# Kernel optimization log

Measured on AMD Instinct MI355X. Metric: run time of the kernel, lower is better.

The kernel has to match this reference:

```python
import jax, jax.numpy as jnp
import numpy as np

N_NODES = 50000
N_EDGES = 600000
N_GRAPHS = 64
D_IN = 128
D_HID = 128
D_LAT = 64
BN_EPS = 1e-5


def setup_inputs() -> dict:
    key = jax.random.key(0)
    ks = jax.random.split(key, 8)
    x = jax.random.normal(ks[0], (N_NODES, D_IN), dtype=jnp.float32)
    edge_index = jax.random.randint(ks[1], (2, N_EDGES), 0, N_NODES, dtype=jnp.int64 if jax.config.jax_enable_x64 else jnp.int32)
    batch = jnp.sort(jax.random.randint(ks[2], (N_NODES,), 0, N_GRAPHS))
    d_cat = 13 * D_IN  # x + (mean,max,min,std) x (identity,amp,att)
    s = 1.0 / np.sqrt(d_cat)
    W0 = jax.random.normal(ks[3], (d_cat, D_HID), dtype=jnp.float32) * s
    W1 = jax.random.normal(ks[4], (13 * D_HID, D_HID), dtype=jnp.float32) * s
    W2 = jax.random.normal(ks[5], (13 * D_HID, D_HID), dtype=jnp.float32) * s
    fcW = jax.random.normal(ks[6], (D_HID, D_LAT), dtype=jnp.float32) * (1.0 / np.sqrt(D_HID))
    return {
        "x": x, "edge_index": edge_index, "batch": batch,
        "W0": W0, "b0": jnp.zeros((D_HID,), jnp.float32),
        "W1": W1, "b1": jnp.zeros((D_HID,), jnp.float32),
        "W2": W2, "b2": jnp.zeros((D_HID,), jnp.float32),
        "bn_gamma": jnp.ones((D_HID,), jnp.float32),
        "bn_beta": jnp.zeros((D_HID,), jnp.float32),
        "fcW": fcW, "fcb": jnp.zeros((D_LAT,), jnp.float32),
    }


def _pna_conv(h, W, b, src, dst, deg, delta):
    # h: [N, d]; messages gathered from source nodes per edge: [E, d]
    m = h[src]
    cnt = jnp.maximum(deg, 1.0)[:, None]
    ssum = jax.ops.segment_sum(m, dst, num_segments=N_NODES)
    mean = ssum / cnt
    ssq = jax.ops.segment_sum(m * m, dst, num_segments=N_NODES)
    std = jnp.sqrt(jnp.maximum(ssq / cnt - mean * mean, 0.0) + 1e-5)
    mx = jax.ops.segment_max(m, dst, num_segments=N_NODES)
    mn = jax.ops.segment_min(m, dst, num_segments=N_NODES)
    has = (deg > 0)[:, None]
    mx = jnp.where(has, mx, 0.0)
    mn = jnp.where(has, mn, 0.0)
    agg = jnp.concatenate([mean, mx, mn, std], axis=-1)  # [N, 4d]
    logd = jnp.log(deg + 1.0)[:, None]
    amp = logd / delta
    att = delta / jnp.maximum(logd, 1e-5)
    feat = jnp.concatenate([h, agg, agg * amp, agg * att], axis=-1)  # [N, 13d]
    return feat @ W + b


def reference(x, edge_index, batch, W0, b0, W1, b1, W2, b2, bn_gamma, bn_beta, fcW, fcb):
    src, dst = edge_index[0], edge_index[1]
    deg = jax.ops.segment_sum(jnp.ones((src.shape[0],), x.dtype), dst, num_segments=N_NODES)
    delta = jnp.mean(jnp.log(deg + 1.0))  # avg log-degree normalizer
    h = jax.nn.relu(_pna_conv(x, W0, b0, src, dst, deg, delta))
    h = jax.nn.relu(_pna_conv(h, W1, b1, src, dst, deg, delta))
    h = jax.nn.relu(_pna_conv(h, W2, b2, src, dst, deg, delta))
    # dropout is identity in eval mode
    pooled = jax.ops.segment_sum(h, batch, num_segments=N_GRAPHS)  # global_add_pool
    mu = jnp.mean(pooled, axis=0)
    var = jnp.var(pooled, axis=0)
    bn = (pooled - mu) / jnp.sqrt(var + BN_EPS) * bn_gamma + bn_beta
    return bn @ fcW + fcb
```

## Files before the change

kernel.cpp:

```cpp
#include <hip/hip_runtime.h>
#include <cstdint>
#include <cstddef>

#define N_NODESC 50000
#define N_PAD    50048
#define N_EDGESC 600000
#define N_GRAPHSC 64
#define D_HIDC   128
#define D_LATC   64
#define D_GS     512
#define D_WROW   1664

typedef unsigned short u16;
typedef unsigned int   u32;

typedef _Float16 f16x8 __attribute__((ext_vector_type(8)));
typedef _Float16 f16x2 __attribute__((ext_vector_type(2)));
typedef float    f32x4 __attribute__((ext_vector_type(4)));
typedef float    f32x2 __attribute__((ext_vector_type(2)));

__device__ __forceinline__ u16 f2h(float f) {
    return __builtin_bit_cast(u16, (_Float16)f);
}
__device__ __forceinline__ float h2f(u16 u) {
    return (float)__builtin_bit_cast(_Float16, u);
}

__device__ __forceinline__ f32x2 pk_add(f32x2 a, f32x2 b) {
    f32x2 d;
    asm("v_pk_add_f32 %0, %1, %2" : "=v"(d) : "v"(a), "v"(b));
    return d;
}
__device__ __forceinline__ f32x2 pk_fma(f32x2 a, f32x2 b, f32x2 c) {
    f32x2 d;
    asm("v_pk_fma_f32 %0, %1, %2, %3" : "=v"(d) : "v"(a), "v"(b), "v"(c));
    return d;
}

__device__ __forceinline__ void gll16(void* lds, const void* g) {
    __builtin_amdgcn_global_load_lds(
        (const __attribute__((address_space(1))) void*)g,
        (__attribute__((address_space(3))) void*)lds, 16, 0, 0);
}

__global__ void __launch_bounds__(256) k_setup(
        const float* __restrict__ x, const float* __restrict__ W0,
        const float* __restrict__ W1, const float* __restrict__ W2,
        const int* __restrict__ batch,
        u16* __restrict__ h, u16* __restrict__ Wt,
        int* __restrict__ zero_base, int nz, int ZB, int* __restrict__ goff) {
    int b = blockIdx.x;
    int t = threadIdx.x;
    if (b < ZB) {
        int i = b * 256 + t;
        if (i < nz) zero_base[i] = 0;
        return;
    }
    b -= ZB;
    if (b < 12500) {
        int i = b * 256 + t;
        float2 v = ((const float2*)x)[i];
        ((u32*)h)[i] = (u32)f2h(v.x) | ((u32)f2h(v.y) << 16);
        return;
    }
    b -= 12500;
    if (b < 2496) {
        int which = b / 832;
        int i = (b % 832) * 256 + t;
        const float* W = (which == 0) ? W0 : (which == 1) ? W1 : W2;
        int k = i / D_HIDC, j = i % D_HIDC;
        Wt[(size_t)which * D_WROW * D_HIDC + (size_t)j * D_WROW + k] = f2h(W[i]);
        return;
    }
    int g = t;
    if (g <= N_GRAPHSC) {
        int lo = 0, hi = N_NODESC;
        while (lo < hi) {
            int mid = (lo + hi) >> 1;
            if (batch[mid] < g) lo = mid + 1; else hi = mid;
        }
        goff[g] = lo;
    }
}

__global__ void k_count(const int* __restrict__ dst, int* __restrict__ deg) {
    int e = blockIdx.x * 256 + threadIdx.x;
    if (e < N_EDGESC) atomicAdd(&deg[dst[e]], 1);
}

__global__ void __launch_bounds__(256) k_scan_part(
        const int* __restrict__ deg, int* __restrict__ bsum,
        float* __restrict__ lsum) {
    __shared__ int s[256];
    __shared__ float ls[256];
    int idx = blockIdx.x * 256 + threadIdx.x;
    int v = (idx < N_NODESC) ? deg[idx] : 0;
    s[threadIdx.x] = v;
    ls[threadIdx.x] = (idx < N_NODESC) ? logf((float)v + 1.0f) : 0.0f;
    __syncthreads();
    for (int o = 128; o > 0; o >>= 1) {
        if (threadIdx.x < o) {
            s[threadIdx.x] += s[threadIdx.x + o];
            ls[threadIdx.x] += ls[threadIdx.x + o];
        }
        __syncthreads();
    }
    if (threadIdx.x == 0) { bsum[blockIdx.x] = s[0]; lsum[blockIdx.x] = ls[0]; }
}

__global__ void __launch_bounds__(256) k_scan_block(
        int* __restrict__ bsum, const float* __restrict__ lsum,
        float* __restrict__ delta_p) {
    __shared__ int s[256];
    __shared__ float ls[256];
    int t = threadIdx.x;
    int v = (t < 196) ? bsum[t] : 0;
    s[t] = v;
    ls[t] = (t < 196) ? lsum[t] : 0.0f;
    __syncthreads();
    for (int o = 1; o < 256; o <<= 1) {
        int add = (t >= o) ? s[t - o] : 0;
        __syncthreads();
        s[t] += add;
        __syncthreads();
    }
    if (t < 196) bsum[t] = s[t] - v;
    for (int o = 128; o > 0; o >>= 1) {
        if (t < o) ls[t] += ls[t + o];
        __syncthreads();
    }
    if (t == 0) delta_p[0] = ls[0] * (1.0f / (float)N_NODESC);
}

__global__ void __launch_bounds__(256) k_scan_final(
        const int* __restrict__ deg, const int* __restrict__ bsum,
        int* __restrict__ row_off) {
    __shared__ int s[256];
    int t = threadIdx.x;
    int idx = blockIdx.x * 256 + t;
    int v = (idx < N_NODESC) ? deg[idx] : 0;
    s[t] = v; __syncthreads();
    for (int o = 1; o < 256; o <<= 1) {
        int add = (t >= o) ? s[t - o] : 0;
        __syncthreads();
        s[t] += add;
        __syncthreads();
    }
    int excl = s[t] - v + bsum[blockIdx.x];
    if (idx < N_NODESC) row_off[idx] = excl;
    if (idx == 0) row_off[N_NODESC] = N_EDGESC;
}

__global__ void k_fill_csr(const int* __restrict__ src, const int* __restrict__ dst,
                           const int* __restrict__ row_off, int* __restrict__ cursor,
                           int* __restrict__ csr_src) {
    int e = blockIdx.x * 256 + threadIdx.x;
    if (e < N_EDGESC) {
        int d = dst[e];
        int pos = row_off[d] + atomicAdd(&cursor[d], 1);
        csr_src[pos] = src[e] << 8;
    }
}


__global__ void __launch_bounds__(256) k_aggregate(
        const u16* __restrict__ h, const int* __restrict__ row_off,
        const int* __restrict__ csr_src, u16* __restrict__ G) {
    int n = blockIdx.x * 4 + (threadIdx.x >> 6);
    if (n >= N_NODESC) return;
    int lane = threadIdx.x & 63;
    int half = lane >> 5, l32 = lane & 31;
    int c4 = 4 * l32;
    u32 c8 = 8u * (u32)l32;
    const char* h8 = (const char*)h;
    int beg = row_off[n], end = row_off[n + 1];
    const _Float16 NEG = (_Float16)(-65504.0f), POS = (_Float16)(65504.0f);
    f32x2 s01 = {0.f, 0.f}, s23 = {0.f, 0.f};
    f32x2 q01 = {0.f, 0.f}, q23 = {0.f, 0.f};
    f16x2 mx01 = {NEG, NEG}, mx23 = {NEG, NEG};
    f16x2 mn01 = {POS, POS}, mn23 = {POS, POS};

    #define PROC(u) { \
        f16x2 p01 = __builtin_bit_cast(f16x2, (u).x); \
        f16x2 p23 = __builtin_bit_cast(f16x2, (u).y); \
        f32x2 c01 = __builtin_convertvector(p01, f32x2); \
        f32x2 c23 = __builtin_convertvector(p23, f32x2); \
        s01 = pk_add(s01, c01); s23 = pk_add(s23, c23); \
        q01 = pk_fma(c01, c01, q01); q23 = pk_fma(c23, c23, q23); \
        mx01 = __builtin_elementwise_max(mx01, p01); \
        mx23 = __builtin_elementwise_max(mx23, p23); \
        mn01 = __builtin_elementwise_min(mn01, p01); \
        mn23 = __builtin_elementwise_min(mn23, p23); }

    int i = beg + half;
    for (; i + 6 < end; i += 8) {
        u32 e0 = (u32)csr_src[i],     e1 = (u32)csr_src[i + 2];
        u32 e2 = (u32)csr_src[i + 4], e3 = (u32)csr_src[i + 6];
        uint2 u0 = *(const uint2*)(h8 + (e0 + c8));
        uint2 u1 = *(const uint2*)(h8 + (e1 + c8));
        uint2 u2 = *(const uint2*)(h8 + (e2 + c8));
        uint2 u3 = *(const uint2*)(h8 + (e3 + c8));
        PROC(u0); PROC(u1); PROC(u2); PROC(u3);
    }
    for (; i < end; i += 2) {
        u32 e0 = (u32)csr_src[i];
        uint2 u0 = *(const uint2*)(h8 + (e0 + c8));
        PROC(u0);
    }
    #undef PROC

    s01.x += __shfl_xor(s01.x, 32); s01.y += __shfl_xor(s01.y, 32);
    s23.x += __shfl_xor(s23.x, 32); s23.y += __shfl_xor(s23.y, 32);
    q01.x += __shfl_xor(q01.x, 32); q01.y += __shfl_xor(q01.y, 32);
    q23.x += __shfl_xor(q23.x, 32); q23.y += __shfl_xor(q23.y, 32);
    #define MRG(v, OP) v = OP(v, \
        __builtin_bit_cast(f16x2, __shfl_xor(__builtin_bit_cast(int, v), 32)))
    MRG(mx01, __builtin_elementwise_max); MRG(mx23, __builtin_elementwise_max);
    MRG(mn01, __builtin_elementwise_min); MRG(mn23, __builtin_elementwise_min);
    #undef MRG

    int d = end - beg;
    float inv = 1.0f / fmaxf((float)d, 1.0f);
    float me0 = s01.x * inv, me1 = s01.y * inv;
    float me2 = s23.x * inv, me3 = s23.y * inv;
    float sd0 = sqrtf(fmaxf(q01.x * inv - me0 * me0, 0.0f) + 1e-5f);
    float sd1 = sqrtf(fmaxf(q01.y * inv - me1 * me1, 0.0f) + 1e-5f);
    float sd2 = sqrtf(fmaxf(q23.x * inv - me2 * me2, 0.0f) + 1e-5f);
    float sd3 = sqrtf(fmaxf(q23.y * inv - me3 * me3, 0.0f) + 1e-5f);
    float fx0 = (float)mx01.x, fx1 = (float)mx01.y;
    float fx2 = (float)mx23.x, fx3 = (float)mx23.y;
    float fn0 = (float)mn01.x, fn1 = (float)mn01.y;
    float fn2 = (float)mn23.x, fn3 = (float)mn23.y;
    if (d == 0) {
        fx0 = fx1 = fx2 = fx3 = 0.0f;
        fn0 = fn1 = fn2 = fn3 = 0.0f;
    }
    u16* base = G + (size_t)n * D_GS;
    #define PK2(a, b) ((u32)f2h(a) | ((u32)f2h(b) << 16))
    if (half == 0) {
        uint2 m; m.x = PK2(me0, me1); m.y = PK2(me2, me3);
        *(uint2*)(base + c4) = m;
        uint2 X; X.x = PK2(fx0, fx1); X.y = PK2(fx2, fx3);
        *(uint2*)(base + 128 + c4) = X;
    } else {
        uint2 N_; N_.x = PK2(fn0, fn1); N_.y = PK2(fn2, fn3);
        *(uint2*)(base + 256 + c4) = N_;
        uint2 S; S.x = PK2(sd0, sd1); S.y = PK2(sd2, sd3);
        *(uint2*)(base + 384 + c4) = S;
    }
    #undef PK2
}

__global__ void __launch_bounds__(256, 2) k_gemm(
        const u16* __restrict__ hin, const u16* __restrict__ G,
        const u16* __restrict__ Wt,
        const int* __restrict__ deg, const float* __restrict__ delta_p,
        const float* __restrict__ bias, u16* __restrict__ hout) {
    __shared__ _Float16 A1[128 * 64];
    __shared__ _Float16 A2[128 * 64];
    __shared__ _Float16 A3[128 * 64];
    __shared__ _Float16 Bt[128 * 64];
    const _Float16* Wf = (const _Float16*)Wt;
    const _Float16* Gf = (const _Float16*)G;
    const _Float16* Hf = (const _Float16*)hin;
    int n0 = blockIdx.x * 128;
    int t = threadIdx.x;
    int w = t >> 6, lane = t & 63;
    int srow8 = lane >> 3, sslot = lane & 7;
    int stg = (sslot ^ srow8) * 8;
    int q4 = lane >> 4, r16 = lane & 15;
    int sx0 = (q4 ^ (lane & 7)) * 8;
    int sx1 = ((q4 + 4) ^ (lane & 7)) * 8;
    int col = lane & 15;

    float delta = delta_p[0];
    float atv[8];
    _Float16 amh[8];
    #pragma unroll
    for (int nt = 0; nt < 8; nt++) {
        int node = n0 + nt * 16 + col;
        float logd = logf((float)deg[node] + 1.0f);
        amh[nt] = (_Float16)(logd / delta);
        atv[nt] = delta / fmaxf(logd, 1e-5f);
    }

    f32x4 acc[2][8], ac3[2][8];
    #pragma unroll
    for (int a = 0; a < 2; a++)
        #pragma unroll
        for (int b = 0; b < 8; b++) {
            acc[a][b] = (f32x4){0.f, 0.f, 0.f, 0.f};
            ac3[a][b] = (f32x4){0.f, 0.f, 0.f, 0.f};
        }

    for (int ki = 0; ki < 10; ki++) {
        int k0 = ki * 64;
        bool sreg = (k0 >= 128);
        __syncthreads();
        #pragma unroll
        for (int r = 0; r < 4; r++) {
            int rr = r * 4 + w;
            const _Float16* wrow = Wf + (size_t)(rr * 8 + srow8) * D_WROW;
            gll16(&A1[rr * 512], wrow + k0 + stg);
        }
        if (sreg) {
            #pragma unroll
            for (int r = 0; r < 4; r++) {
                int rr = r * 4 + w;
                const _Float16* wrow = Wf + (size_t)(rr * 8 + srow8) * D_WROW;
                gll16(&A2[rr * 512], wrow + 512 + k0 + stg);
                gll16(&A3[rr * 512], wrow + 1024 + k0 + stg);
            }
        }
        #pragma unroll
        for (int q = 0; q < 4; q++) {
            int rr = q * 4 + w;
            int row = n0 + rr * 8 + srow8;
            const _Float16* bsrc = (!sreg)
                ? Hf + (size_t)row * D_HIDC + k0 + stg
                : Gf + (size_t)row * D_GS + (k0 - 128) + stg;
            gll16(&Bt[rr * 512], bsrc);
        }
        __syncthreads();
        f16x8 a00 = *(const f16x8*)&A1[(w * 32 + r16) * 64 + sx0];
        f16x8 a01 = *(const f16x8*)&A1[(w * 32 + r16) * 64 + sx1];
        f16x8 a10 = *(const f16x8*)&A1[(w * 32 + 16 + r16) * 64 + sx0];
        f16x8 a11 = *(const f16x8*)&A1[(w * 32 + 16 + r16) * 64 + sx1];
        if (!sreg) {
            #pragma unroll
            for (int nt = 0; nt < 8; nt++) {
                f16x8 b0 = *(const f16x8*)&Bt[(nt * 16 + r16) * 64 + sx0];
                f16x8 b1 = *(const f16x8*)&Bt[(nt * 16 + r16) * 64 + sx1];
                acc[0][nt] = __builtin_amdgcn_mfma_f32_16x16x32_f16(a00, b0, acc[0][nt], 0, 0, 0);
                acc[1][nt] = __builtin_amdgcn_mfma_f32_16x16x32_f16(a10, b0, acc[1][nt], 0, 0, 0);
                acc[0][nt] = __builtin_amdgcn_mfma_f32_16x16x32_f16(a01, b1, acc[0][nt], 0, 0, 0);
                acc[1][nt] = __builtin_amdgcn_mfma_f32_16x16x32_f16(a11, b1, acc[1][nt], 0, 0, 0);
            }
        } else {
            f16x8 w2a0 = *(const f16x8*)&A2[(w * 32 + r16) * 64 + sx0];
            f16x8 w2a1 = *(const f16x8*)&A2[(w * 32 + r16) * 64 + sx1];
            f16x8 w2b0 = *(const f16x8*)&A2[(w * 32 + 16 + r16) * 64 + sx0];
            f16x8 w2b1 = *(const f16x8*)&A2[(w * 32 + 16 + r16) * 64 + sx1];
            f16x8 w3a0 = *(const f16x8*)&A3[(w * 32 + r16) * 64 + sx0];
            f16x8 w3a1 = *(const f16x8*)&A3[(w * 32 + r16) * 64 + sx1];
            f16x8 w3b0 = *(const f16x8*)&A3[(w * 32 + 16 + r16) * 64 + sx0];
            f16x8 w3b1 = *(const f16x8*)&A3[(w * 32 + 16 + r16) * 64 + sx1];
            #pragma unroll
            for (int nt = 0; nt < 8; nt++) {
                f16x8 b0 = *(const f16x8*)&Bt[(nt * 16 + r16) * 64 + sx0];
                f16x8 b1 = *(const f16x8*)&Bt[(nt * 16 + r16) * 64 + sx1];
                f16x8 bm0 = b0 * amh[nt];
                f16x8 bm1 = b1 * amh[nt];
                acc[0][nt] = __builtin_amdgcn_mfma_f32_16x16x32_f16(a00, b0, acc[0][nt], 0, 0, 0);
                acc[1][nt] = __builtin_amdgcn_mfma_f32_16x16x32_f16(a10, b0, acc[1][nt], 0, 0, 0);
                acc[0][nt] = __builtin_amdgcn_mfma_f32_16x16x32_f16(a01, b1, acc[0][nt], 0, 0, 0);
                acc[1][nt] = __builtin_amdgcn_mfma_f32_16x16x32_f16(a11, b1, acc[1][nt], 0, 0, 0);
                acc[0][nt] = __builtin_amdgcn_mfma_f32_16x16x32_f16(w2a0, bm0, acc[0][nt], 0, 0, 0);
                acc[1][nt] = __builtin_amdgcn_mfma_f32_16x16x32_f16(w2b0, bm0, acc[1][nt], 0, 0, 0);
                acc[0][nt] = __builtin_amdgcn_mfma_f32_16x16x32_f16(w2a1, bm1, acc[0][nt], 0, 0, 0);
                acc[1][nt] = __builtin_amdgcn_mfma_f32_16x16x32_f16(w2b1, bm1, acc[1][nt], 0, 0, 0);
                ac3[0][nt] = __builtin_amdgcn_mfma_f32_16x16x32_f16(w3a0, b0, ac3[0][nt], 0, 0, 0);
                ac3[1][nt] = __builtin_amdgcn_mfma_f32_16x16x32_f16(w3b0, b0, ac3[1][nt], 0, 0, 0);
                ac3[0][nt] = __builtin_amdgcn_mfma_f32_16x16x32_f16(w3a1, b1, ac3[0][nt], 0, 0, 0);
                ac3[1][nt] = __builtin_amdgcn_mfma_f32_16x16x32_f16(w3b1, b1, ac3[1][nt], 0, 0, 0);
            }
        }
    }
    int rowq = q4 * 4;
    #pragma unroll
    for (int nt = 0; nt < 8; nt++) {
        int node = n0 + nt * 16 + col;
        float at = atv[nt];
        #pragma unroll
        for (int mt = 0; mt < 2; mt++) {
            int jb = w * 32 + mt * 16 + rowq;
            f32x4 v = acc[mt][nt], v3 = ac3[mt][nt];
            ushort4 o;
            o.x = f2h(fmaxf(v.x + at * v3.x + bias[jb], 0.0f));
            o.y = f2h(fmaxf(v.y + at * v3.y + bias[jb + 1], 0.0f));
            o.z = f2h(fmaxf(v.z + at * v3.z + bias[jb + 2], 0.0f));
            o.w = f2h(fmaxf(v.w + at * v3.w + bias[jb + 3], 0.0f));
            *(ushort4*)&hout[(size_t)node * D_HIDC + jb] = o;
        }
    }
}


__global__ void __launch_bounds__(256) k_pool(
        const u16* __restrict__ h, const int* __restrict__ goff,
        float* __restrict__ pooled) {
    __shared__ float sm[256];
    int g = blockIdx.x >> 2, s = blockIdx.x & 3;
    int gb = goff[g], ge = goff[g + 1];
    int len = ge - gb;
    int q = (len + 3) >> 2;
    int nb = gb + s * q;
    int ne = min(nb + q, ge);
    int t = threadIdx.x;
    int j = t & 127, half = t >> 7;
    float acc = 0.0f;
    for (int n = nb + half; n < ne; n += 2)
        acc += h2f(h[(size_t)n * D_HIDC + j]);
    sm[t] = acc; __syncthreads();
    if (t < 128) {
        float v = sm[t] + sm[t + 128];
        atomicAdd(&pooled[g * D_HIDC + j], v);
    }
}

__global__ void __launch_bounds__(128) k_bn_fc(
        const float* __restrict__ pooled, const float* __restrict__ gamma,
        const float* __restrict__ beta, const float* __restrict__ fcW,
        const float* __restrict__ fcb, float* __restrict__ out) {
    __shared__ float bn[D_HIDC];
    int g = blockIdx.x, t = threadIdx.x;
    float s = 0.f, q = 0.f;
    for (int gg = 0; gg < N_GRAPHSC; gg++) {
        float v = pooled[gg * D_HIDC + t];
        s += v; q += v * v;
    }
    float mu = s * (1.0f / N_GRAPHSC);
    float var = q * (1.0f / N_GRAPHSC) - mu * mu;
    float inv = 1.0f / sqrtf(var + 1e-5f);
    bn[t] = (pooled[g * D_HIDC + t] - mu) * inv * gamma[t] + beta[t];
    __syncthreads();
    if (t < D_LATC) {
        float accum = fcb[t];
        for (int j = 0; j < D_HIDC; j++) accum += bn[j] * fcW[j * D_LATC + t];
        out[g * D_LATC + t] = accum;
    }
}


extern "C" void kernel_launch(void* const* d_in, const int* in_sizes, int n_in,
                              void* d_out, int out_size, void* d_ws, size_t ws_size,
                              hipStream_t stream) {
    const float* x     = (const float*)d_in[0];
    const int*   ei    = (const int*)d_in[1];
    const int*   batch = (const int*)d_in[2];
    const float* W0 = (const float*)d_in[3];
    const float* b0 = (const float*)d_in[4];
    const float* W1 = (const float*)d_in[5];
    const float* b1 = (const float*)d_in[6];
    const float* W2 = (const float*)d_in[7];
    const float* b2 = (const float*)d_in[8];
    const float* gamma = (const float*)d_in[9];
    const float* beta  = (const float*)d_in[10];
    const float* fcW   = (const float*)d_in[11];
    const float* fcb   = (const float*)d_in[12];
    float* out = (float*)d_out;
    const int* srcv = ei;
    const int* dstv = ei + N_EDGESC;

    char* p = (char*)d_ws;
    auto alloc = [&](size_t bytes) -> char* {
        char* r = p;
        p += (bytes + 255) & ~(size_t)255;
        return r;
    };
    int*   deg_cnt = (int*)alloc((size_t)N_PAD * 4);
    int*   cursor  = (int*)alloc((size_t)N_NODESC * 4);
    float* delta_p = (float*)alloc(4);
    float* pooled  = (float*)alloc((size_t)N_GRAPHSC * D_HIDC * 4);
    char*  zero_end = p;
    int*   row_off = (int*)alloc((size_t)(N_NODESC + 1) * 4);
    int*   goff    = (int*)alloc((size_t)(N_GRAPHSC + 1) * 4);
    int*   bsum    = (int*)alloc(256 * 4);
    float* lsum    = (float*)alloc(256 * 4);
    int*   csr_src = (int*)alloc((size_t)N_EDGESC * 4);
    u16*   Wt      = (u16*)alloc((size_t)3 * D_WROW * D_HIDC * 2);
    u16*   hA      = (u16*)alloc((size_t)N_PAD * D_HIDC * 2);
    u16*   hB      = (u16*)alloc((size_t)N_PAD * D_HIDC * 2);
    u16*   G       = (u16*)alloc((size_t)N_PAD * D_GS * 2);

    int nz = (int)((zero_end - (char*)deg_cnt) / 4);
    int ZB = (nz + 255) / 256;
    int setup_grid = ZB + 12500 + 2496 + 1;
    k_setup<<<setup_grid, 256, 0, stream>>>(x, W0, W1, W2, batch,
                                            hB, Wt, deg_cnt, nz, ZB, goff);
    k_count<<<(N_EDGESC + 255) / 256, 256, 0, stream>>>(dstv, deg_cnt);
    k_scan_part<<<196, 256, 0, stream>>>(deg_cnt, bsum, lsum);
    k_scan_block<<<1, 256, 0, stream>>>(bsum, lsum, delta_p);
    k_scan_final<<<196, 256, 0, stream>>>(deg_cnt, bsum, row_off);
    k_fill_csr<<<(N_EDGESC + 255) / 256, 256, 0, stream>>>(srcv, dstv, row_off, cursor, csr_src);

    const float* bs[3] = {b0, b1, b2};
    const u16* h_in[3]  = {hB, hA, hB};
    u16*       h_out[3] = {hA, hB, hA};
    size_t wsz = (size_t)D_WROW * D_HIDC;
    for (int l = 0; l < 3; l++) {
        k_aggregate<<<(N_NODESC + 3) / 4, 256, 0, stream>>>(
            h_in[l], row_off, csr_src, G);
        k_gemm<<<N_PAD / 128, 256, 0, stream>>>(
            h_in[l], G, Wt + (size_t)l * wsz, deg_cnt, delta_p, bs[l], h_out[l]);
    }
    k_pool<<<4 * N_GRAPHSC, 256, 0, stream>>>(h_out[2], goff, pooled);
    k_bn_fc<<<N_GRAPHSC, 128, 0, stream>>>(pooled, gamma, beta, fcW, fcb, out);
}
```

Baseline: 396.2 us.

## Double-buffer GEMM LDS tiles with async prefetch and halved K-step

The fused PNA GEMM kernel now uses two LDS buffers with 32-wide K tiles instead of one 64-wide tile. The next tile's global-to-LDS loads are issued before computing the current one, and explicit vmcnt waits plus raw barriers replace the __syncthreads pairs, so load latency overlaps MFMA work. It also raises wave priority during compute. The cost is more loop iterations and barriers, plus fragile hand-counted vmcnt values that must match the number of loads issued per stage.

```diff
diff --git a/kernel.cpp b/kernel.cpp
--- a/kernel.cpp
+++ b/kernel.cpp
@@ -256,22 +256,29 @@
         const u16* __restrict__ Wt,
         const int* __restrict__ deg, const float* __restrict__ delta_p,
         const float* __restrict__ bias, u16* __restrict__ hout) {
-    __shared__ _Float16 A1[128 * 64];
-    __shared__ _Float16 A2[128 * 64];
-    __shared__ _Float16 A3[128 * 64];
-    __shared__ _Float16 Bt[128 * 64];
+    __shared__ _Float16 A1[2][128 * 32];
+    __shared__ _Float16 A2[2][128 * 32];
+    __shared__ _Float16 A3[2][128 * 32];
+    __shared__ _Float16 Bt[2][128 * 32];
     const _Float16* Wf = (const _Float16*)Wt;
     const _Float16* Gf = (const _Float16*)G;
     const _Float16* Hf = (const _Float16*)hin;
     int n0 = blockIdx.x * 128;
     int t = threadIdx.x;
     int w = t >> 6, lane = t & 63;
-    int srow8 = lane >> 3, sslot = lane & 7;
-    int stg = (sslot ^ srow8) * 8;
+    int srow4 = lane >> 2, schk = lane & 3;
+    int scol = (schk ^ (srow4 & 3)) * 8;
     int q4 = lane >> 4, r16 = lane & 15;
-    int sx0 = (q4 ^ (lane & 7)) * 8;
-    int sx1 = ((q4 + 4) ^ (lane & 7)) * 8;
-    int col = lane & 15;
+    int sx = (q4 ^ (r16 & 3)) * 8;
+    int col = r16;
+    int iA0 = w, iA1 = 4 + w;
+
+    const _Float16* wA0 = Wf + (size_t)(iA0 * 16 + srow4) * D_WROW + scol;
+    const _Float16* wA1 = Wf + (size_t)(iA1 * 16 + srow4) * D_WROW + scol;
+    const _Float16* hB0 = Hf + (size_t)(n0 + iA0 * 16 + srow4) * D_HIDC + scol;
+    const _Float16* hB1 = Hf + (size_t)(n0 + iA1 * 16 + srow4) * D_HIDC + scol;
+    const _Float16* gB0 = Gf + (size_t)(n0 + iA0 * 16 + srow4) * D_GS + scol - 128;
+    const _Float16* gB1 = Gf + (size_t)(n0 + iA1 * 16 + srow4) * D_GS + scol - 128;
 
     float delta = delta_p[0];
     float atv[8];
@@ -293,79 +300,69 @@
             ac3[a][b] = (f32x4){0.f, 0.f, 0.f, 0.f};
         }
 
-    for (int ki = 0; ki < 10; ki++) {
-        int k0 = ki * 64;
-        bool sreg = (k0 >= 128);
-        __syncthreads();
-        #pragma unroll
-        for (int r = 0; r < 4; r++) {
-            int rr = r * 4 + w;
-            const _Float16* wrow = Wf + (size_t)(rr * 8 + srow8) * D_WROW;
-            gll16(&A1[rr * 512], wrow + k0 + stg);
-        }
-        if (sreg) {
-            #pragma unroll
-            for (int r = 0; r < 4; r++) {
-                int rr = r * 4 + w;
-                const _Float16* wrow = Wf + (size_t)(rr * 8 + srow8) * D_WROW;
-                gll16(&A2[rr * 512], wrow + 512 + k0 + stg);
-                gll16(&A3[rr * 512], wrow + 1024 + k0 + stg);
-            }
-        }
-        #pragma unroll
-        for (int q = 0; q < 4; q++) {
-            int rr = q * 4 + w;
-            int row = n0 + rr * 8 + srow8;
-            const _Float16* bsrc = (!sreg)
-                ? Hf + (size_t)row * D_HIDC + k0 + stg
-                : Gf + (size_t)row * D_GS + (k0 - 128) + stg;
-            gll16(&Bt[rr * 512], bsrc);
-        }
-        __syncthreads();
-        f16x8 a00 = *(const f16x8*)&A1[(w * 32 + r16) * 64 + sx0];
-        f16x8 a01 = *(const f16x8*)&A1[(w * 32 + r16) * 64 + sx1];
-        f16x8 a10 = *(const f16x8*)&A1[(w * 32 + 16 + r16) * 64 + sx0];
-        f16x8 a11 = *(const f16x8*)&A1[(w * 32 + 16 + r16) * 64 + sx1];
-        if (!sreg) {
-            #pragma unroll
-            for (int nt = 0; nt < 8; nt++) {
-                f16x8 b0 = *(const f16x8*)&Bt[(nt * 16 + r16) * 64 + sx0];
-                f16x8 b1 = *(const f16x8*)&Bt[(nt * 16 + r16) * 64 + sx1];
-                acc[0][nt] = __builtin_amdgcn_mfma_f32_16x16x32_f16(a00, b0, acc[0][nt], 0, 0, 0);
-                acc[1][nt] = __builtin_amdgcn_mfma_f32_16x16x32_f16(a10, b0, acc[1][nt], 0, 0, 0);
-                acc[0][nt] = __builtin_amdgcn_mfma_f32_16x16x32_f16(a01, b1, acc[0][nt], 0, 0, 0);
-                acc[1][nt] = __builtin_amdgcn_mfma_f32_16x16x32_f16(a11, b1, acc[1][nt], 0, 0, 0);
-            }
-        } else {
-            f16x8 w2a0 = *(const f16x8*)&A2[(w * 32 + r16) * 64 + sx0];
-            f16x8 w2a1 = *(const f16x8*)&A2[(w * 32 + r16) * 64 + sx1];
-            f16x8 w2b0 = *(const f16x8*)&A2[(w * 32 + 16 + r16) * 64 + sx0];
-            f16x8 w2b1 = *(const f16x8*)&A2[(w * 32 + 16 + r16) * 64 + sx1];
-            f16x8 w3a0 = *(const f16x8*)&A3[(w * 32 + r16) * 64 + sx0];
-            f16x8 w3a1 = *(const f16x8*)&A3[(w * 32 + r16) * 64 + sx1];
-            f16x8 w3b0 = *(const f16x8*)&A3[(w * 32 + 16 + r16) * 64 + sx0];
-            f16x8 w3b1 = *(const f16x8*)&A3[(w * 32 + 16 + r16) * 64 + sx1];
-            #pragma unroll
-            for (int nt = 0; nt < 8; nt++) {
-                f16x8 b0 = *(const f16x8*)&Bt[(nt * 16 + r16) * 64 + sx0];
-                f16x8 b1 = *(const f16x8*)&Bt[(nt * 16 + r16) * 64 + sx1];
-                f16x8 bm0 = b0 * amh[nt];
-                f16x8 bm1 = b1 * amh[nt];
-                acc[0][nt] = __builtin_amdgcn_mfma_f32_16x16x32_f16(a00, b0, acc[0][nt], 0, 0, 0);
-                acc[1][nt] = __builtin_amdgcn_mfma_f32_16x16x32_f16(a10, b0, acc[1][nt], 0, 0, 0);
-                acc[0][nt] = __builtin_amdgcn_mfma_f32_16x16x32_f16(a01, b1, acc[0][nt], 0, 0, 0);
-                acc[1][nt] = __builtin_amdgcn_mfma_f32_16x16x32_f16(a11, b1, acc[1][nt], 0, 0, 0);
-                acc[0][nt] = __builtin_amdgcn_mfma_f32_16x16x32_f16(w2a0, bm0, acc[0][nt], 0, 0, 0);
-                acc[1][nt] = __builtin_amdgcn_mfma_f32_16x16x32_f16(w2b0, bm0, acc[1][nt], 0, 0, 0);
-                acc[0][nt] = __builtin_amdgcn_mfma_f32_16x16x32_f16(w2a1, bm1, acc[0][nt], 0, 0, 0);
-                acc[1][nt] = __builtin_amdgcn_mfma_f32_16x16x32_f16(w2b1, bm1, acc[1][nt], 0, 0, 0);
-                ac3[0][nt] = __builtin_amdgcn_mfma_f32_16x16x32_f16(w3a0, b0, ac3[0][nt], 0, 0, 0);
-                ac3[1][nt] = __builtin_amdgcn_mfma_f32_16x16x32_f16(w3b0, b0, ac3[1][nt], 0, 0, 0);
-                ac3[0][nt] = __builtin_amdgcn_mfma_f32_16x16x32_f16(w3a1, b1, ac3[0][nt], 0, 0, 0);
-                ac3[1][nt] = __builtin_amdgcn_mfma_f32_16x16x32_f16(w3b1, b1, ac3[1][nt], 0, 0, 0);
-            }
-        }
-    }
+    #define STAGE(KI, BUF) do { \
+        gll16(&A1[BUF][iA0 * 512], wA0 + (KI) * 32); \
+        gll16(&A1[BUF][iA1 * 512], wA1 + (KI) * 32); \
+        if ((KI) >= 4) { \
+            gll16(&A2[BUF][iA0 * 512], wA0 + 512 + (KI) * 32); \
+            gll16(&A2[BUF][iA1 * 512], wA1 + 512 + (KI) * 32); \
+            gll16(&A3[BUF][iA0 * 512], wA0 + 1024 + (KI) * 32); \
+            gll16(&A3[BUF][iA1 * 512], wA1 + 1024 + (KI) * 32); \
+            gll16(&Bt[BUF][iA0 * 512], gB0 + (KI) * 32); \
+            gll16(&Bt[BUF][iA1 * 512], gB1 + (KI) * 32); \
+        } else { \
+            gll16(&Bt[BUF][iA0 * 512], hB0 + (KI) * 32); \
+            gll16(&Bt[BUF][iA1 * 512], hB1 + (KI) * 32); \
+        } \
+    } while (0)
+
+    #define COMPUTE(KI, BUF) do { \
+        f16x8 a00 = *(const f16x8*)&A1[BUF][(w * 32 + r16) * 32 + sx]; \
+        f16x8 a10 = *(const f16x8*)&A1[BUF][(w * 32 + 16 + r16) * 32 + sx]; \
+        if ((KI) < 4) { \
+            _Pragma("unroll") \
+            for (int nt = 0; nt < 8; nt++) { \
+                f16x8 b0 = *(const f16x8*)&Bt[BUF][(nt * 16 + r16) * 32 + sx]; \
+                acc[0][nt] = __builtin_amdgcn_mfma_f32_16x16x32_f16(a00, b0, acc[0][nt], 0, 0, 0); \
+                acc[1][nt] = __builtin_amdgcn_mfma_f32_16x16x32_f16(a10, b0, acc[1][nt], 0, 0, 0); \
+            } \
+        } else { \
+            f16x8 w2l = *(const f16x8*)&A2[BUF][(w * 32 + r16) * 32 + sx]; \
+            f16x8 w2h = *(const f16x8*)&A2[BUF][(w * 32 + 16 + r16) * 32 + sx]; \
+            f16x8 w3l = *(const f16x8*)&A3[BUF][(w * 32 + r16) * 32 + sx]; \
+            f16x8 w3h = *(const f16x8*)&A3[BUF][(w * 32 + 16 + r16) * 32 + sx]; \
+            _Pragma("unroll") \
+            for (int nt = 0; nt < 8; nt++) { \
+                f16x8 b0 = *(const f16x8*)&Bt[BUF][(nt * 16 + r16) * 32 + sx]; \
+                f16x8 bm = b0 * amh[nt]; \
+                acc[0][nt] = __builtin_amdgcn_mfma_f32_16x16x32_f16(a00, b0, acc[0][nt], 0, 0, 0); \
+                acc[1][nt] = __builtin_amdgcn_mfma_f32_16x16x32_f16(a10, b0, acc[1][nt], 0, 0, 0); \
+                acc[0][nt] = __builtin_amdgcn_mfma_f32_16x16x32_f16(w2l, bm, acc[0][nt], 0, 0, 0); \
+                acc[1][nt] = __builtin_amdgcn_mfma_f32_16x16x32_f16(w2h, bm, acc[1][nt], 0, 0, 0); \
+                ac3[0][nt] = __builtin_amdgcn_mfma_f32_16x16x32_f16(w3l, b0, ac3[0][nt], 0, 0, 0); \
+                ac3[1][nt] = __builtin_amdgcn_mfma_f32_16x16x32_f16(w3h, b0, ac3[1][nt], 0, 0, 0); \
+            } \
+        } \
+    } while (0)
+
+    asm volatile("s_waitcnt vmcnt(0)" ::: "memory");
+    STAGE(0, 0);
+    #pragma unroll
+    for (int ki = 0; ki < 20; ki++) {
+        int cb = ki & 1, nb = cb ^ 1;
+        if (ki < 19) STAGE(ki + 1, nb);
+        if (ki == 19)        asm volatile("s_waitcnt vmcnt(0)" ::: "memory");
+        else if (ki + 1 < 4) asm volatile("s_waitcnt vmcnt(4)" ::: "memory");
+        else                 asm volatile("s_waitcnt vmcnt(8)" ::: "memory");
+        asm volatile("s_barrier" ::: "memory");
+        __builtin_amdgcn_s_setprio(1);
+        COMPUTE(ki, cb);
+        __builtin_amdgcn_s_setprio(0);
+        asm volatile("s_barrier" ::: "memory");
+    }
+    #undef STAGE
+    #undef COMPUTE
+
     int rowq = q4 * 4;
     #pragma unroll
     for (int nt = 0; nt < 8; nt++) {
```

Result: no change. 403.6 us (+1.9%).
